# Kernel optimization log

Hardware: AMD Instinct MI355X
Metric: run time of the kernel (lower is better)

## Reference

```python
import jax, jax.numpy as jnp
import numpy as np

NUM_HEADS = 16
EPS = 1e-6
ROPE_THETA = 10000.0


def _rmsnorm_fp32(x, w):
    # RMSNorm computed in fp32, scale by learned weight (per head_dim)
    xf = x.astype(jnp.float32)
    var = jnp.mean(xf * xf, axis=-1, keepdims=True)
    return (xf * jax.lax.rsqrt(var + EPS) * w.astype(jnp.float32)).astype(x.dtype)


def _rope_3d_angles(T, H, W, head_dim):
    # split head_dim across (t,h,w) axes; all parts even
    dh = 2 * ((head_dim // 3) // 2)
    dw = dh
    dt = head_dim - dh - dw

    def axis_ang(L, d):
        inv = 1.0 / (ROPE_THETA ** (jnp.arange(0, d, 2, dtype=jnp.float32) / d))
        return jnp.arange(L, dtype=jnp.float32)[:, None] * inv[None, :]  # [L, d//2]

    at = axis_ang(T, dt)  # [T, dt/2]
    ah = axis_ang(H, dh)  # [H, dh/2]
    aw = axis_ang(W, dw)  # [W, dw/2]
    # broadcast to [T,H,W, head_dim//2] then flatten to [N, head_dim//2]
    at_g = jnp.broadcast_to(at[:, None, None, :], (T, H, W, dt // 2))
    ah_g = jnp.broadcast_to(ah[None, :, None, :], (T, H, W, dh // 2))
    aw_g = jnp.broadcast_to(aw[None, None, :, :], (T, H, W, dw // 2))
    ang = jnp.concatenate([at_g, ah_g, aw_g], axis=-1).reshape(T * H * W, head_dim // 2)
    return jnp.cos(ang), jnp.sin(ang)


def _apply_rope(x, cos, sin):
    # x: [B,Hh,N,D]; cos/sin: [N, D/2]; interleaved complex-pair rotation
    xr = x[..., 0::2]
    xi = x[..., 1::2]
    c = cos[None, None, :, :]
    s = sin[None, None, :, :]
    out_r = xr * c - xi * s
    out_i = xr * s + xi * c
    return jnp.stack([out_r, out_i], axis=-1).reshape(x.shape)


def setup_inputs() -> dict:
    key = jax.random.key(0)
    ks = jax.random.split(key, 7)
    dim, hd = 2048, 128
    x = jax.random.normal(ks[0], (1, 2048, dim), dtype=jnp.float32)
    qkv_w = jax.random.normal(ks[1], (3 * dim, dim), dtype=jnp.float32) * (dim ** -0.5)
    qkv_b = jax.random.normal(ks[2], (3 * dim,), dtype=jnp.float32) * 0.02
    proj_w = jax.random.normal(ks[3], (dim, dim), dtype=jnp.float32) * (dim ** -0.5)
    proj_b = jax.random.normal(ks[4], (dim,), dtype=jnp.float32) * 0.02
    q_norm_w = jnp.ones((hd,), dtype=jnp.float32)
    k_norm_w = jnp.ones((hd,), dtype=jnp.float32)
    return {"x": x, "qkv_w": qkv_w, "qkv_b": qkv_b, "proj_w": proj_w,
            "proj_b": proj_b, "q_norm_w": q_norm_w, "k_norm_w": k_norm_w,
            "t_dim": 8, "h_dim": 16, "w_dim": 16}


def reference(x, qkv_w, qkv_b, proj_w, proj_b, q_norm_w, k_norm_w, t_dim, h_dim, w_dim):
    B, N, C = x.shape
    Hh = NUM_HEADS
    D = C // Hh
    scale = D ** -0.5
    # QKV projection (torch Linear: x @ W.T + b)
    qkv = x @ qkv_w.T + qkv_b                      # [B,N,3C]
    qkv = qkv.reshape(B, N, 3, Hh, D).transpose(2, 0, 3, 1, 4)  # [3,B,Hh,N,D]
    q, k, v = qkv[0], qkv[1], qkv[2]
    q = _rmsnorm_fp32(q, q_norm_w)
    k = _rmsnorm_fp32(k, k_norm_w)
    cos, sin = _rope_3d_angles(t_dim, h_dim, w_dim, D)
    q = _apply_rope(q, cos, sin)
    k = _apply_rope(k, cos, sin)
    # SDPA (non-causal)
    scores = jnp.einsum('bhqd,bhkd->bhqk', q, k) * scale
    attn = jax.nn.softmax(scores, axis=-1)
    out = jnp.einsum('bhqk,bhkd->bhqd', attn, v)   # [B,Hh,N,D]
    out = out.transpose(0, 2, 1, 3).reshape(B, N, C)
    return out @ proj_w.T + proj_b
```

## Files before the change

### kernel.cpp

```cpp
#include <hip/hip_runtime.h>
#include <hip/hip_bf16.h>
#include <cstdint>
#include <cstddef>

typedef __attribute__((ext_vector_type(8))) short bf16x8;
typedef __attribute__((ext_vector_type(4))) float f32x4;
typedef __attribute__((ext_vector_type(16))) float f32x16;

#define AS1 __attribute__((address_space(1)))
#define AS3 __attribute__((address_space(3)))

__device__ __forceinline__ void gload_lds16(const void* g, void* l) {
  __builtin_amdgcn_global_load_lds((const AS1 void*)g, (AS3 void*)l, 16, 0, 0);
}

__device__ __forceinline__ unsigned short f2bf(float x) {
  __hip_bfloat16 h = __float2bfloat16(x);
  return __builtin_bit_cast(unsigned short, h);
}
__device__ __forceinline__ float bf2f(unsigned short u) {
  return __builtin_bit_cast(float, (unsigned int)u << 16);
}

__global__ __launch_bounds__(256) void k_cvt_bf16(const float* __restrict__ in,
                                                  unsigned short* __restrict__ out,
                                                  int n4) {
  int i = blockIdx.x * 256 + threadIdx.x;
  const int stride = gridDim.x * 256;
  for (; i < n4; i += stride) {
    float4 v = reinterpret_cast<const float4*>(in)[i];
    ushort4 o;
    o.x = f2bf(v.x); o.y = f2bf(v.y); o.z = f2bf(v.z); o.w = f2bf(v.w);
    reinterpret_cast<ushort4*>(out)[i] = o;
  }
}

__global__ __launch_bounds__(256) void k_rope_tab(float* __restrict__ cosT,
                                                  float* __restrict__ sinT,
                                                  const int* __restrict__ hdim,
                                                  const int* __restrict__ wdim) {
  int idx = blockIdx.x * 256 + threadIdx.x;
  if (idx >= 2048 * 64) return;
  const int n = idx >> 6, j = idx & 63;
  const int H = *hdim, W = *wdim;
  const int w = n % W;
  const int rem = n / W;
  const int h = rem % H;
  const int t = rem / H;
  float pos, i2, d;
  if (j < 22)      { pos = (float)t; i2 = (float)(2 * j);        d = 44.f; }
  else if (j < 43) { pos = (float)h; i2 = (float)(2 * (j - 22)); d = 42.f; }
  else             { pos = (float)w; i2 = (float)(2 * (j - 43)); d = 42.f; }
  const float ang = pos * powf(10000.0f, -i2 / d);
  cosT[idx] = cosf(ang);
  sinT[idx] = sinf(ang);
}

__global__ __launch_bounds__(256, 2) void k_gemmQKV(const unsigned short* __restrict__ A,
                                                    const unsigned short* __restrict__ B,
                                                    const float* __restrict__ bias,
                                                    unsigned short* __restrict__ C,
                                                    int M, int N, int K) {
  __shared__ __align__(16) char lds[81920];
  const int tid = threadIdx.x;
  const int lane = tid & 63;
  const int wid = tid >> 6;
  const int wr = wid >> 1, wc = wid & 1;

  const int xcd = blockIdx.x & 7;
  const int t = blockIdx.x >> 3;
  const int bx = xcd * 4 + (t & 3);
  const int by = t >> 2;
  const int row0 = by * 128, col0 = bx * 192;
  const int NT = K >> 6;

  auto stageA = [&](int grow0, int kcol0, char* slot) {
#pragma unroll
    for (int r = 0; r < 2; ++r) {
      const int off = r * 4096 + tid * 16;
      const int pair = off >> 7;
      const int un = (off & 127) ^ ((pair & 7) << 4);
      const int grow = pair * 2 + (un >> 6);
      gload_lds16(A + (size_t)(grow0 + grow) * K + kcol0 + ((un & 63) >> 1),
                  slot + r * 4096 + wid * 1024);
    }
  };
  auto stageB = [&](int grow0, int kcol0, char* slot) {
#pragma unroll
    for (int r = 0; r < 3; ++r) {
      const int off = r * 4096 + tid * 16;
      const int pair = off >> 7;
      const int un = (off & 127) ^ ((pair & 7) << 4);
      const int grow = pair * 2 + (un >> 6);
      gload_lds16(B + (size_t)(grow0 + grow) * K + kcol0 + ((un & 63) >> 1),
                  slot + r * 4096 + wid * 1024);
    }
  };
  auto frag = [&](const char* slot, int r, int kb) -> bf16x8 {
    return *reinterpret_cast<const bf16x8*>(
        slot + (r >> 1) * 128 + ((((r & 1) << 6) + kb) ^ (((r >> 1) & 7) << 4)));
  };

  f32x4 acc[4][6];
#pragma unroll
  for (int i = 0; i < 4; ++i)
#pragma unroll
    for (int j = 0; j < 6; ++j) acc[i][j] = (f32x4){0.f, 0.f, 0.f, 0.f};

  stageA(row0, 0,  lds);
  stageB(col0, 0,  lds + 16384);
  stageA(row0, 32, lds + 8192);
  stageB(col0, 32, lds + 28672);
  asm volatile("s_waitcnt vmcnt(5)" ::: "memory");
  __builtin_amdgcn_s_barrier();

  const int kb = (lane >> 4) << 4;
  for (int j = 0; j < NT; ++j) {
    const int b = j & 1, bp = b ^ 1;
    const char* base = lds + b * 40960;
    char* pbase = lds + bp * 40960;
    const bool pf = (j + 1 < NT);
    const int kn = (j + 1) * 64;
    bf16x8 af[4], bq[6];

#pragma unroll
    for (int fr = 0; fr < 4; ++fr) af[fr] = frag(base, wr * 64 + fr * 16 + (lane & 15), kb);
#pragma unroll
    for (int fc = 0; fc < 6; ++fc) bq[fc] = frag(base + 16384, wc * 96 + fc * 16 + (lane & 15), kb);
    if (pf) { stageA(row0, kn, pbase); stageB(col0, kn, pbase + 16384); }
    if (pf) asm volatile("s_waitcnt vmcnt(5)" ::: "memory");
    else    asm volatile("s_waitcnt vmcnt(0)" ::: "memory");
    __builtin_amdgcn_s_barrier();
    __builtin_amdgcn_s_setprio(1);
#pragma unroll
    for (int fr = 0; fr < 4; ++fr)
#pragma unroll
      for (int fc = 0; fc < 6; ++fc)
        acc[fr][fc] = __builtin_amdgcn_mfma_f32_16x16x32_bf16(af[fr], bq[fc], acc[fr][fc], 0, 0, 0);
    __builtin_amdgcn_s_setprio(0);
    __builtin_amdgcn_s_barrier();

#pragma unroll
    for (int fr = 0; fr < 4; ++fr) af[fr] = frag(base + 8192, wr * 64 + fr * 16 + (lane & 15), kb);
#pragma unroll
    for (int fc = 0; fc < 6; ++fc) bq[fc] = frag(base + 28672, wc * 96 + fc * 16 + (lane & 15), kb);
    if (pf) { stageA(row0, kn + 32, pbase + 8192); stageB(col0, kn + 32, pbase + 28672); }
    if (pf) asm volatile("s_waitcnt vmcnt(5)" ::: "memory");
    __builtin_amdgcn_s_barrier();
    __builtin_amdgcn_s_setprio(1);
#pragma unroll
    for (int fr = 0; fr < 4; ++fr)
#pragma unroll
      for (int fc = 0; fc < 6; ++fc)
        acc[fr][fc] = __builtin_amdgcn_mfma_f32_16x16x32_bf16(af[fr], bq[fc], acc[fr][fc], 0, 0, 0);
    __builtin_amdgcn_s_setprio(0);
    __builtin_amdgcn_s_barrier();
  }

#pragma unroll
  for (int fr = 0; fr < 4; ++fr)
#pragma unroll
    for (int fc = 0; fc < 6; ++fc) {
      const int col = col0 + wc * 96 + fc * 16 + (lane & 15);
      const float bv = bias[col];
#pragma unroll
      for (int jj = 0; jj < 4; ++jj) {
        const int row = row0 + wr * 64 + fr * 16 + (lane >> 4) * 4 + jj;
        C[(size_t)row * N + col] = f2bf(acc[fr][fc][jj] + bv);
      }
    }
}

__global__ __launch_bounds__(256) void k_gemm_bt_sk(const unsigned short* __restrict__ A,
                                                    const unsigned short* __restrict__ B,
                                                    float* __restrict__ Cp,
                                                    int M, int N, int K, int KS) {
  __shared__ __align__(16) unsigned short As[128 * 32];
  __shared__ __align__(16) unsigned short Bs[128 * 32];
  const int lane = threadIdx.x & 63;
  const int wid  = threadIdx.x >> 6;
  const int wr = wid >> 1, wc = wid & 1;
  const int rowA0 = blockIdx.y * 128;
  const int rowB0 = blockIdx.x * 128;
  const int k0 = blockIdx.z * KS;

  f32x4 acc[4][4];
#pragma unroll
  for (int i = 0; i < 4; ++i)
#pragma unroll
    for (int j = 0; j < 4; ++j) acc[i][j] = (f32x4){0.f, 0.f, 0.f, 0.f};

  for (int kt = k0; kt < k0 + KS; kt += 32) {
#pragma unroll
    for (int i = 0; i < 2; ++i) {
      const int c = i * 4 + wid;
      const int off = c * 1024 + lane * 16;
      const int row = off >> 6;
      const int col = (off & 63) >> 1;
      gload_lds16(A + (size_t)(rowA0 + row) * K + kt + col, (char*)As + c * 1024);
      gload_lds16(B + (size_t)(rowB0 + row) * K + kt + col, (char*)Bs + c * 1024);
    }
    __syncthreads();
    bf16x8 af[4], bfr[4];
#pragma unroll
    for (int mi = 0; mi < 4; ++mi)
      af[mi] = *reinterpret_cast<const bf16x8*>(
          &As[(wr * 64 + mi * 16 + (lane & 15)) * 32 + (lane >> 4) * 8]);
#pragma unroll
    for (int ni = 0; ni < 4; ++ni)
      bfr[ni] = *reinterpret_cast<const bf16x8*>(
          &Bs[(wc * 64 + ni * 16 + (lane & 15)) * 32 + (lane >> 4) * 8]);
#pragma unroll
    for (int mi = 0; mi < 4; ++mi)
#pragma unroll
      for (int ni = 0; ni < 4; ++ni)
        acc[mi][ni] = __builtin_amdgcn_mfma_f32_16x16x32_bf16(af[mi], bfr[ni], acc[mi][ni], 0, 0, 0);
    __syncthreads();
  }

  float* Cz = Cp + (size_t)blockIdx.z * M * N;
#pragma unroll
  for (int mi = 0; mi < 4; ++mi)
#pragma unroll
    for (int ni = 0; ni < 4; ++ni) {
      const int col = rowB0 + wc * 64 + ni * 16 + (lane & 15);
#pragma unroll
      for (int j = 0; j < 4; ++j) {
        const int row = rowA0 + wr * 64 + mi * 16 + (lane >> 4) * 4 + j;
        Cz[(size_t)row * N + col] = acc[mi][ni][j];
      }
    }
}

__global__ __launch_bounds__(256) void k_addbias(const float* __restrict__ Cp,
                                                 const float* __restrict__ bias,
                                                 float* __restrict__ out) {
  const int i = blockIdx.x * 256 + threadIdx.x;
  const float4 a = reinterpret_cast<const float4*>(Cp)[i];
  const float4 b = reinterpret_cast<const float4*>(Cp + 2048ull * 2048)[i];
  const float4 bv = reinterpret_cast<const float4*>(bias)[i & 511];
  float4 o;
  o.x = a.x + b.x + bv.x; o.y = a.y + b.y + bv.y;
  o.z = a.z + b.z + bv.z; o.w = a.w + b.w + bv.w;
  reinterpret_cast<float4*>(out)[i] = o;
}

__global__ __launch_bounds__(256) void k_qk_post(const unsigned short* __restrict__ qkv,
                                                 const float* __restrict__ qw,
                                                 const float* __restrict__ kw,
                                                 const float* __restrict__ cosT,
                                                 const float* __restrict__ sinT,
                                                 unsigned short* __restrict__ qo,
                                                 unsigned short* __restrict__ ko) {
  const int lane = threadIdx.x & 63;
  const int wid = threadIdx.x >> 6;
  const int pair = blockIdx.x * 4 + wid;
  const int n = pair >> 4, h = pair & 15;
  const float c = cosT[n * 64 + lane];
  const float s = sinT[n * 64 + lane];
#pragma unroll
  for (int sq = 0; sq < 2; ++sq) {
    const unsigned short* src = qkv + (size_t)n * 6144 + sq * 2048 + h * 128;
    const unsigned int vp = reinterpret_cast<const unsigned int*>(src)[lane];
    const float vx = bf2f((unsigned short)(vp & 0xffff));
    const float vy = bf2f((unsigned short)(vp >> 16));
    float ss = vx * vx + vy * vy;
#pragma unroll
    for (int m = 1; m < 64; m <<= 1) ss += __shfl_xor(ss, m, 64);
    const float r = rsqrtf(ss * (1.0f / 128.0f) + 1e-6f);
    float2 wv = reinterpret_cast<const float2*>(sq == 0 ? qw : kw)[lane];
    const float xr = vx * r * wv.x;
    const float xi = vy * r * wv.y;
    float orr = xr * c - xi * s;
    float oi  = xr * s + xi * c;
    if (sq == 0) { orr *= 0.08838834764831845f; oi *= 0.08838834764831845f; }
    unsigned short* dst = (sq == 0 ? qo : ko) + ((size_t)h * 2048 + n) * 128 + 2 * lane;
    const unsigned int pk = (unsigned int)f2bf(orr) | ((unsigned int)f2bf(oi) << 16);
    *reinterpret_cast<unsigned int*>(dst) = pk;
  }
}

__global__ __launch_bounds__(256) void k_v_tr(const unsigned short* __restrict__ qkv,
                                              unsigned short* __restrict__ vt2) {
  __shared__ __align__(16) unsigned short tile[64][136];
  const int h = blockIdx.y;
  const int n0 = blockIdx.x * 64;
  const int t = threadIdx.x;
  {
    const int row = t >> 2;
    const int c0 = (t & 3) * 32;
    const unsigned short* src = qkv + (size_t)(n0 + row) * 6144 + 4096 + h * 128 + c0;
#pragma unroll
    for (int j = 0; j < 32; j += 8)
      *reinterpret_cast<bf16x8*>(&tile[row][c0 + j]) =
          *reinterpret_cast<const bf16x8*>(src + j);
  }
  __syncthreads();
#pragma unroll
  for (int g4 = 0; g4 < 4; ++g4) {
    const int g = g4 * 256 + t;
    const int c = g >> 8;
    const int dblk = (g >> 6) & 3;
    const int p = g & 63;
    const int d = dblk * 32 + (p & 31);
    const int hi = p >> 5;
    bf16x8 o;
#pragma unroll
    for (int e = 0; e < 8; ++e) o[e] = (short)tile[c * 16 + hi * 8 + e][d];
    const size_t oidx = ((((size_t)h * 128 + (n0 >> 4) + c) * 4 + dblk) * 64 + p) * 8;
    *reinterpret_cast<bf16x8*>(vt2 + oidx) = o;
  }
}

__global__ __launch_bounds__(256) void k_fattn(const unsigned short* __restrict__ q,
                                               const unsigned short* __restrict__ k,
                                               const unsigned short* __restrict__ vt2,
                                               unsigned short* __restrict__ Onorm,
                                               float* __restrict__ lseb) {
  __shared__ __align__(16) unsigned short Ks[3][64 * 128];
  __shared__ __align__(16) unsigned short Ps[4][32][68];
  const int lane = threadIdx.x & 63;
  const int wid = threadIdx.x >> 6;
  const int hi2 = lane >> 5;
  const int ql = lane & 31;
  const int bid = blockIdx.x;
  const int h = bid & 15;
  const int qb = (bid >> 4) & 15;
  const int ksp = bid >> 8;
  const int q0 = qb * 128 + wid * 32;
  const int kbase = ksp * 1024;

  auto stageK = [&](int buf, int kt2) {
#pragma unroll
    for (int r = 0; r < 4; ++r) {
      const int off = r * 4096 + (wid * 64 + lane) * 16;
      const int row = off >> 8;
      const int colb = (off & 255) ^ ((row & 15) << 4);
      gload_lds16(k + ((size_t)h * 2048 + kbase + kt2 * 64 + row) * 128 + (colb >> 1),
                  (char*)Ks[buf] + r * 4096 + wid * 1024);
    }
  };

  bf16x8 qf[8];
  {
    const unsigned short* qp = q + ((size_t)h * 2048 + q0 + ql) * 128 + hi2 * 8;
#pragma unroll
    for (int c = 0; c < 8; ++c) qf[c] = *reinterpret_cast<const bf16x8*>(qp + c * 16);
  }
  f32x16 O[4];
#pragma unroll
  for (int i = 0; i < 4; ++i)
#pragma unroll
    for (int j = 0; j < 16; ++j) O[i][j] = 0.f;
  float m = -1e30f, l = 0.f;

  stageK(0, 0);
  stageK(1, 1);
  asm volatile("s_waitcnt vmcnt(4)" ::: "memory");
  __builtin_amdgcn_s_barrier();

  const int kswz = (lane & 15) << 4;
  for (int kt = 0; kt < 16; ++kt) {
    const int cur = kt % 3;

    f32x16 s0, s1;
#pragma unroll
    for (int j = 0; j < 16; ++j) { s0[j] = 0.f; s1[j] = 0.f; }
    __builtin_amdgcn_s_setprio(1);
#pragma unroll
    for (int c = 0; c < 8; ++c) {
      bf16x8 a0 = *reinterpret_cast<const bf16x8*>(
          (const char*)Ks[cur] + ql * 256 + ((c * 32 + hi2 * 16) ^ kswz));
      s0 = __builtin_amdgcn_mfma_f32_32x32x16_bf16(a0, qf[c], s0, 0, 0, 0);
    }
#pragma unroll
    for (int c = 0; c < 8; ++c) {
      bf16x8 a1 = *reinterpret_cast<const bf16x8*>(
          (const char*)Ks[cur] + (32 + ql) * 256 + ((c * 32 + hi2 * 16) ^ kswz));
      s1 = __builtin_amdgcn_mfma_f32_32x32x16_bf16(a1, qf[c], s1, 0, 0, 0);
    }
    __builtin_amdgcn_s_setprio(0);

    float mt = s0[0];
#pragma unroll
    for (int j = 1; j < 16; ++j) mt = fmaxf(mt, s0[j]);
#pragma unroll
    for (int j = 0; j < 16; ++j) mt = fmaxf(mt, s1[j]);
    mt = fmaxf(mt, __shfl_xor(mt, 32, 64));

    if (!__all(mt <= m + 8.0f)) {
      const float mn = fmaxf(m, mt);
      const float al = __expf(m - mn);
      m = mn;
      l *= al;
#pragma unroll
      for (int i = 0; i < 4; ++i)
#pragma unroll
        for (int j = 0; j < 16; ++j) O[i][j] *= al;
    }
    float rs = 0.f;
#pragma unroll
    for (int j = 0; j < 16; ++j) {
      s0[j] = __expf(s0[j] - m); rs += s0[j];
      s1[j] = __expf(s1[j] - m); rs += s1[j];
    }
    rs += __shfl_xor(rs, 32, 64);
    l += rs;

#pragma unroll
    for (int a = 0; a < 4; ++a) {
      uint2 w0, w1;
      w0.x = (unsigned)f2bf(s0[a * 4 + 0]) | ((unsigned)f2bf(s0[a * 4 + 1]) << 16);
      w0.y = (unsigned)f2bf(s0[a * 4 + 2]) | ((unsigned)f2bf(s0[a * 4 + 3]) << 16);
      w1.x = (unsigned)f2bf(s1[a * 4 + 0]) | ((unsigned)f2bf(s1[a * 4 + 1]) << 16);
      w1.y = (unsigned)f2bf(s1[a * 4 + 2]) | ((unsigned)f2bf(s1[a * 4 + 3]) << 16);
      *reinterpret_cast<uint2*>(&Ps[wid][ql][a * 8 + hi2 * 4]) = w0;
      *reinterpret_cast<uint2*>(&Ps[wid][ql][32 + a * 8 + hi2 * 4]) = w1;
    }
    bf16x8 pf[4];
#pragma unroll
    for (int c2 = 0; c2 < 4; ++c2) {
      uint2 u0 = *reinterpret_cast<const uint2*>(&Ps[wid][ql][c2 * 16 + hi2 * 8]);
      uint2 u1 = *reinterpret_cast<const uint2*>(&Ps[wid][ql][c2 * 16 + hi2 * 8 + 4]);
      union { uint4 u; bf16x8 v; } pu;
      pu.u.x = u0.x; pu.u.y = u0.y; pu.u.z = u1.x; pu.u.w = u1.y;
      pf[c2] = pu.v;
    }

    const int cg0 = (kbase >> 4) + kt * 4;
    __builtin_amdgcn_s_setprio(1);
#pragma unroll
    for (int dblk = 0; dblk < 4; ++dblk) {
#pragma unroll
      for (int c2 = 0; c2 < 4; ++c2) {
        bf16x8 va = *reinterpret_cast<const bf16x8*>(
            vt2 + ((((size_t)h * 128 + cg0 + c2) * 4 + dblk) * 64 + lane) * 8);
        O[dblk] = __builtin_amdgcn_mfma_f32_32x32x16_bf16(va, pf[c2], O[dblk], 0, 0, 0);
      }
    }
    __builtin_amdgcn_s_setprio(0);

    if (kt + 2 < 16) stageK((kt + 2) % 3, kt + 2);
    if (kt + 1 < 16) {
      asm volatile("s_waitcnt vmcnt(4)" ::: "memory");
      __builtin_amdgcn_s_barrier();
    }
  }

  const float rl = 1.0f / l;
  const int n = q0 + ql;
  unsigned short* ob = Onorm + (((size_t)(ksp * 16 + h) * 2048) + n) * 128;
#pragma unroll
  for (int dblk = 0; dblk < 4; ++dblk)
#pragma unroll
    for (int a = 0; a < 4; ++a) {
      uint2 w;
      w.x = (unsigned)f2bf(O[dblk][a * 4 + 0] * rl) | ((unsigned)f2bf(O[dblk][a * 4 + 1] * rl) << 16);
      w.y = (unsigned)f2bf(O[dblk][a * 4 + 2] * rl) | ((unsigned)f2bf(O[dblk][a * 4 + 3] * rl) << 16);
      *reinterpret_cast<uint2*>(ob + dblk * 32 + a * 8 + hi2 * 4) = w;
    }
  if (hi2 == 0)
    lseb[(size_t)(ksp * 16 + h) * 2048 + n] = m + logf(l);
}

__global__ __launch_bounds__(256) void k_merge(const unsigned short* __restrict__ Onorm,
                                               const float* __restrict__ lseb,
                                               unsigned short* __restrict__ att) {
  const int idx = blockIdx.x * 256 + threadIdx.x;
  const int n = idx >> 8;
  const int r = idx & 255;
  const int h = r >> 4;
  const int d0 = (r & 15) * 8;
  const float l0 = lseb[(size_t)h * 2048 + n];
  const float l1 = lseb[(size_t)(16 + h) * 2048 + n];
  const float M = fmaxf(l0, l1);
  float w0 = __expf(l0 - M), w1 = __expf(l1 - M);
  const float inv = 1.0f / (w0 + w1);
  w0 *= inv; w1 *= inv;
  const bf16x8 o0 = *reinterpret_cast<const bf16x8*>(
      Onorm + ((size_t)h * 2048 + n) * 128 + d0);
  const bf16x8 o1 = *reinterpret_cast<const bf16x8*>(
      Onorm + ((size_t)(16 + h) * 2048 + n) * 128 + d0);
  bf16x8 o;
#pragma unroll
  for (int e = 0; e < 8; ++e)
    o[e] = (short)f2bf(bf2f((unsigned short)o0[e]) * w0 + bf2f((unsigned short)o1[e]) * w1);
  *reinterpret_cast<bf16x8*>(att + (size_t)n * 2048 + h * 128 + d0) = o;
}

extern "C" void kernel_launch(void* const* d_in, const int* in_sizes, int n_in,
                              void* d_out, int out_size, void* d_ws, size_t ws_size,
                              hipStream_t stream) {
  (void)in_sizes; (void)n_in; (void)out_size; (void)ws_size;
  const float* x      = (const float*)d_in[0];
  const float* qkv_w  = (const float*)d_in[1];
  const float* qkv_b  = (const float*)d_in[2];
  const float* proj_w = (const float*)d_in[3];
  const float* proj_b = (const float*)d_in[4];
  const float* q_nw   = (const float*)d_in[5];
  const float* k_nw   = (const float*)d_in[6];
  const int* h_dim    = (const int*)d_in[8];
  const int* w_dim    = (const int*)d_in[9];
  float* out = (float*)d_out;

  char* ws = (char*)d_ws;
  size_t off = 0;
  auto carve = [&](size_t bytes) -> void* {
    void* p = ws + off;
    off += (bytes + 255) & ~(size_t)255;
    return p;
  };
  unsigned short* x_bf   = (unsigned short*)carve(2048ull * 2048 * 2);
  unsigned short* w1_bf  = (unsigned short*)carve(6144ull * 2048 * 2);
  unsigned short* w2_bf  = (unsigned short*)carve(2048ull * 2048 * 2);
  unsigned short* qkvb   = (unsigned short*)carve(2048ull * 6144 * 2);
  unsigned short* q_bf   = (unsigned short*)carve(16ull * 2048 * 128 * 2);
  unsigned short* k_bf   = (unsigned short*)carve(16ull * 2048 * 128 * 2);
  unsigned short* vt2_bf = (unsigned short*)carve(16ull * 2048 * 128 * 2);
  unsigned short* att_bf = (unsigned short*)carve(2048ull * 2048 * 2);
  unsigned short* on_bf  = (unsigned short*)carve(2ull * 16 * 2048 * 128 * 2);
  float*          lseb   = (float*)carve(2ull * 16 * 2048 * 4);
  float*          projp  = (float*)carve(2ull * 2048 * 2048 * 4);
  float*          cosT   = (float*)carve(2048ull * 64 * 4);
  float*          sinT   = (float*)carve(2048ull * 64 * 4);

  hipLaunchKernelGGL(k_cvt_bf16, dim3(2048), dim3(256), 0, stream, x, x_bf, 2048 * 2048 / 4);
  hipLaunchKernelGGL(k_cvt_bf16, dim3(2048), dim3(256), 0, stream, qkv_w, w1_bf, 6144 * 2048 / 4);
  hipLaunchKernelGGL(k_cvt_bf16, dim3(2048), dim3(256), 0, stream, proj_w, w2_bf, 2048 * 2048 / 4);
  hipLaunchKernelGGL(k_rope_tab, dim3(512), dim3(256), 0, stream, cosT, sinT, h_dim, w_dim);
  hipLaunchKernelGGL(k_gemmQKV, dim3(512), dim3(256), 0, stream,
                     x_bf, w1_bf, qkv_b, qkvb, 2048, 6144, 2048);
  hipLaunchKernelGGL(k_qk_post, dim3(8192), dim3(256), 0, stream,
                     qkvb, q_nw, k_nw, cosT, sinT, q_bf, k_bf);
  hipLaunchKernelGGL(k_v_tr, dim3(32, 16), dim3(256), 0, stream, qkvb, vt2_bf);
  hipLaunchKernelGGL(k_fattn, dim3(512), dim3(256), 0, stream,
                     q_bf, k_bf, vt2_bf, on_bf, lseb);
  hipLaunchKernelGGL(k_merge, dim3(2048), dim3(256), 0, stream, on_bf, lseb, att_bf);
  hipLaunchKernelGGL(k_gemm_bt_sk, dim3(16, 16, 2), dim3(256), 0, stream,
                     att_bf, w2_bf, projp, 2048, 2048, 2048, 1024);
  hipLaunchKernelGGL(k_addbias, dim3(4096), dim3(256), 0, stream, projp, proj_b, out);
}
```

Baseline: 204.2 us.

## Stage V tiles through LDS and build P fragments in registers via permlane swap

The attention kernel now loads V tiles into LDS with async global-to-LDS copies, double-buffered alongside K, instead of reading V straight from global memory inside the PV MFMA loop. The softmax probabilities are packed with v_cvt_pk_bf16_f32 and rearranged across lane halves with v_permlane32_swap, which removes the per-wave LDS round trip through the Ps buffer. K buffering drops from triple to double, each prefetch is issued at the top of the iteration, and the loop now waits on vmcnt(0). This trades a shallower prefetch depth and a full wait per iteration for fewer LDS writes and reads and more regular V access.

```diff
diff --git a/kernel.cpp b/kernel.cpp
--- a/kernel.cpp
+++ b/kernel.cpp
@@ -20,6 +20,14 @@
 }
 __device__ __forceinline__ float bf2f(unsigned short u) {
   return __builtin_bit_cast(float, (unsigned int)u << 16);
+}
+__device__ __forceinline__ unsigned cvtpk(float a, float b) {
+  unsigned r;
+  asm("v_cvt_pk_bf16_f32 %0, %1, %2" : "=v"(r) : "v"(a), "v"(b));
+  return r;
+}
+__device__ __forceinline__ void pswap(unsigned& x, unsigned& y) {
+  asm volatile("v_permlane32_swap_b32 %0, %1" : "+v"(x), "+v"(y));
 }
 
 __global__ __launch_bounds__(256) void k_cvt_bf16(const float* __restrict__ in,
@@ -317,8 +325,8 @@
                                                const unsigned short* __restrict__ vt2,
                                                unsigned short* __restrict__ Onorm,
                                                float* __restrict__ lseb) {
-  __shared__ __align__(16) unsigned short Ks[3][64 * 128];
-  __shared__ __align__(16) unsigned short Ps[4][32][68];
+  __shared__ __align__(16) unsigned short Ks[2][64 * 128];
+  __shared__ __align__(16) unsigned short Vs[2][64 * 128];
   const int lane = threadIdx.x & 63;
   const int wid = threadIdx.x >> 6;
   const int hi2 = lane >> 5;
@@ -340,6 +348,13 @@
                   (char*)Ks[buf] + r * 4096 + wid * 1024);
     }
   };
+  auto stageV = [&](int buf, int kt2) {
+    const unsigned short* vbase = vt2 + ((size_t)h * 128 + (kbase >> 4) + kt2 * 4) * 2048;
+#pragma unroll
+    for (int r = 0; r < 4; ++r)
+      gload_lds16(vbase + r * 2048 + (wid * 64 + lane) * 8,
+                  (char*)Vs[buf] + r * 4096 + wid * 1024);
+  };
 
   bf16x8 qf[8];
   {
@@ -355,13 +370,15 @@
   float m = -1e30f, l = 0.f;
 
   stageK(0, 0);
-  stageK(1, 1);
-  asm volatile("s_waitcnt vmcnt(4)" ::: "memory");
+  stageV(0, 0);
+  asm volatile("s_waitcnt vmcnt(0)" ::: "memory");
   __builtin_amdgcn_s_barrier();
 
   const int kswz = (lane & 15) << 4;
   for (int kt = 0; kt < 16; ++kt) {
-    const int cur = kt % 3;
+    const int cur = kt & 1;
+    const bool pf = (kt + 1 < 16);
+    if (pf) { stageK(cur ^ 1, kt + 1); stageV(cur ^ 1, kt + 1); }
 
     f32x16 s0, s1;
 #pragma unroll
@@ -407,42 +424,38 @@
     rs += __shfl_xor(rs, 32, 64);
     l += rs;
 
-#pragma unroll
-    for (int a = 0; a < 4; ++a) {
-      uint2 w0, w1;
-      w0.x = (unsigned)f2bf(s0[a * 4 + 0]) | ((unsigned)f2bf(s0[a * 4 + 1]) << 16);
-      w0.y = (unsigned)f2bf(s0[a * 4 + 2]) | ((unsigned)f2bf(s0[a * 4 + 3]) << 16);
-      w1.x = (unsigned)f2bf(s1[a * 4 + 0]) | ((unsigned)f2bf(s1[a * 4 + 1]) << 16);
-      w1.y = (unsigned)f2bf(s1[a * 4 + 2]) | ((unsigned)f2bf(s1[a * 4 + 3]) << 16);
-      *reinterpret_cast<uint2*>(&Ps[wid][ql][a * 8 + hi2 * 4]) = w0;
-      *reinterpret_cast<uint2*>(&Ps[wid][ql][32 + a * 8 + hi2 * 4]) = w1;
-    }
-    bf16x8 pf[4];
-#pragma unroll
-    for (int c2 = 0; c2 < 4; ++c2) {
-      uint2 u0 = *reinterpret_cast<const uint2*>(&Ps[wid][ql][c2 * 16 + hi2 * 8]);
-      uint2 u1 = *reinterpret_cast<const uint2*>(&Ps[wid][ql][c2 * 16 + hi2 * 8 + 4]);
-      union { uint4 u; bf16x8 v; } pu;
-      pu.u.x = u0.x; pu.u.y = u0.y; pu.u.z = u1.x; pu.u.w = u1.y;
-      pf[c2] = pu.v;
-    }
-
-    const int cg0 = (kbase >> 4) + kt * 4;
+    bf16x8 pfr[4];
+#pragma unroll
+    for (int half = 0; half < 2; ++half) {
+      const f32x16& sv = half ? s1 : s0;
+      unsigned a[8];
+#pragma unroll
+      for (int j2 = 0; j2 < 8; ++j2) a[j2] = cvtpk(sv[2 * j2], sv[2 * j2 + 1]);
+      pswap(a[0], a[2]);
+      pswap(a[1], a[3]);
+      pswap(a[4], a[6]);
+      pswap(a[5], a[7]);
+      union { uint4 u; bf16x8 v; } p0, p1;
+      p0.u.x = a[0]; p0.u.y = a[1]; p0.u.z = a[2]; p0.u.w = a[3];
+      p1.u.x = a[4]; p1.u.y = a[5]; p1.u.z = a[6]; p1.u.w = a[7];
+      pfr[half * 2 + 0] = p0.v;
+      pfr[half * 2 + 1] = p1.v;
+    }
+
     __builtin_amdgcn_s_setprio(1);
 #pragma unroll
     for (int dblk = 0; dblk < 4; ++dblk) {
 #pragma unroll
       for (int c2 = 0; c2 < 4; ++c2) {
         bf16x8 va = *reinterpret_cast<const bf16x8*>(
-            vt2 + ((((size_t)h * 128 + cg0 + c2) * 4 + dblk) * 64 + lane) * 8);
-        O[dblk] = __builtin_amdgcn_mfma_f32_32x32x16_bf16(va, pf[c2], O[dblk], 0, 0, 0);
+            (const char*)Vs[cur] + ((c2 * 4 + dblk) * 64 + lane) * 16);
+        O[dblk] = __builtin_amdgcn_mfma_f32_32x32x16_bf16(va, pfr[c2], O[dblk], 0, 0, 0);
       }
     }
     __builtin_amdgcn_s_setprio(0);
 
-    if (kt + 2 < 16) stageK((kt + 2) % 3, kt + 2);
-    if (kt + 1 < 16) {
-      asm volatile("s_waitcnt vmcnt(4)" ::: "memory");
+    if (pf) {
+      asm volatile("s_waitcnt vmcnt(0)" ::: "memory");
       __builtin_amdgcn_s_barrier();
     }
   }
```

Result: faster. 186.3 us (-8.8%).
